# Kernel tuning notes

Measured on AMD Instinct MI355X. Metric: run time of the kernel, lower is better.

The kernel has to match this reference:

```python
import jax, jax.numpy as jnp
import numpy as np

B, C, N, F_, HID = 512, 3, 128, 256, 128  # batch, channels, nodes(=in_dim), num_f(=seq), gru hidden


def setup_inputs() -> dict:
    key = jax.random.key(0)
    ks = jax.random.split(key, 12)
    s = 0.05
    inp = {
        "X": jax.random.normal(ks[0], (B, N, F_), jnp.float32),
        "H": jax.random.uniform(ks[1], (B, C, N, N), jnp.float32),
        "weight": jnp.full((1, 1), 10.0, jnp.float32),        # nn.init.constant_(weight, 10)
        "soft": jnp.full((C,), 1.0 / C, jnp.float32),          # nn.init.constant_(soft, 1/C)
        "w_ih_f": jax.random.normal(ks[2], (3 * HID, N), jnp.float32) * s,
        "w_hh_f": jax.random.normal(ks[3], (3 * HID, HID), jnp.float32) * s,
        "b_ih_f": jax.random.normal(ks[4], (3 * HID,), jnp.float32) * s,
        "b_hh_f": jax.random.normal(ks[5], (3 * HID,), jnp.float32) * s,
        "w_ih_b": jax.random.normal(ks[6], (3 * HID, N), jnp.float32) * s,
        "w_hh_b": jax.random.normal(ks[7], (3 * HID, HID), jnp.float32) * s,
        "b_ih_b": jax.random.normal(ks[8], (3 * HID,), jnp.float32) * s,
        "b_hh_b": jax.random.normal(ks[9], (3 * HID,), jnp.float32) * s,
        "bn_gamma": jnp.ones((F_,), jnp.float32),
        "bn_beta": jnp.zeros((F_,), jnp.float32),
    }
    return inp


def _gru_dir(xs, w_ih, w_hh, b_ih, b_hh):
    # xs: [T, B, in] -> ys: [T, B, HID]; torch GRU cell equations
    def cell(h, x):
        gi = x @ w_ih.T + b_ih
        gh = h @ w_hh.T + b_hh
        i_r, i_z, i_n = jnp.split(gi, 3, axis=-1)
        h_r, h_z, h_n = jnp.split(gh, 3, axis=-1)
        r = jax.nn.sigmoid(i_r + h_r)
        z = jax.nn.sigmoid(i_z + h_z)
        n = jnp.tanh(i_n + r * h_n)
        h_new = (1.0 - z) * n + z * h
        return h_new, h_new
    h0 = jnp.zeros((xs.shape[1], w_hh.shape[1]), xs.dtype)
    _, ys = jax.lax.scan(cell, h0, xs)
    return ys


def reference(X, H, weight, soft, w_ih_f, w_hh_f, b_ih_f, b_hh_f,
              w_ih_b, w_hh_b, b_ih_b, b_hh_b, bn_gamma, bn_beta):
    n = X.shape[1]
    I = jnp.eye(n, dtype=X.dtype)
    # norm(): zero the diagonal, add identity, symmetric D^-1/2 H D^-1/2 (all C channels at once)
    Hn = H * (1.0 - I) + I                              # [B,C,N,N]
    deg = jnp.sum(Hn, axis=-1)                          # [B,C,N]
    dinv = deg ** -0.5
    Hn = dinv[..., :, None] * Hn * dinv[..., None, :]
    # gcn_conv across all features/channels in one einsum; weight is a 1x1 scalar
    HX = jnp.einsum('bcnm,bmf->bcnf', Hn, X) * weight[0, 0]
    Xc = jnp.sum(jax.nn.leaky_relu(HX, 0.01) * soft[None, :, None, None], axis=1)  # [B,N,F]
    # per1 -> [B, F, N]; GRU batch_first with seq_len=F, input=N
    xs = Xc.transpose(2, 0, 1)                          # [T=F, B, N]
    yf = _gru_dir(xs, w_ih_f, w_hh_f, b_ih_f, b_hh_f)
    yb = _gru_dir(xs[::-1], w_ih_b, w_hh_b, b_ih_b, b_hh_b)[::-1]
    y = jnp.concatenate([yf, yb], axis=-1).transpose(1, 0, 2)  # [B, F, 2*HID]

    # BatchNorm1d(num_f), training-mode batch stats over (batch, length) per channel F
    mean = jnp.mean(y, axis=(0, 2), keepdims=True)
    var = jnp.var(y, axis=(0, 2), keepdims=True)
    y = bn_gamma[None, :, None] * (y - mean) / jnp.sqrt(var + 1e-5) + bn_beta[None, :, None]
    # per2 -> [B, 2*HID, F]
    return y.transpose(0, 2, 1)
```

## Files before the change

kernel.cpp:

```cpp
#include <hip/hip_runtime.h>

typedef short s8v  __attribute__((ext_vector_type(8)));
typedef float f4v  __attribute__((ext_vector_type(4)));

#define B_   512
#define C_   3
#define N_   128
#define F_   256
#define T_   256
#define HID_ 128
#define G3_  384

__device__ __forceinline__ ushort f2bf(float f) {
  union { float f; unsigned u; } v; v.f = f;
  return (ushort)((v.u + 0x7FFFu + ((v.u >> 16) & 1u)) >> 16);
}
__device__ __forceinline__ float bf2f(ushort h) {
  union { unsigned u; float f; } v; v.u = ((unsigned)h) << 16;
  return v.f;
}
__device__ __forceinline__ float rcp_(float x) { return __builtin_amdgcn_rcpf(x); }
__device__ __forceinline__ float sigm(float x) { return rcp_(1.0f + __expf(-x)); }
__device__ __forceinline__ float tanh_(float x) { return 2.0f * rcp_(1.0f + __expf(-2.0f * x)) - 1.0f; }

#define LDS_BARRIER() asm volatile("s_waitcnt lgkmcnt(0)\n\ts_barrier" ::: "memory")

__global__ void k_wcvt(const float* __restrict__ a, const float* __restrict__ b,
                       const float* __restrict__ c, const float* __restrict__ d,
                       ushort* __restrict__ o) {
  int i = blockIdx.x * 256 + threadIdx.x;
  const float* src = (i < 49152) ? a : (i < 98304) ? b : (i < 147456) ? c : d;
  o[i] = f2bf(src[i % 49152]);
}

__global__ void k_dinv(const float* __restrict__ H, float* __restrict__ dinv) {
  const int bc = blockIdx.x;
  const int lane = threadIdx.x & 63, w = threadIdx.x >> 6;
  const float* Hm = H + (size_t)bc * N_ * N_;
  for (int r = w * 32; r < w * 32 + 32; ++r) {
    float a = Hm[(size_t)r * N_ + lane];
    float b = Hm[(size_t)r * N_ + 64 + lane];
    if (lane == r) a = 1.0f;
    if (64 + lane == r) b = 1.0f;
    float s = a + b;
    #pragma unroll
    for (int o = 32; o; o >>= 1) s += __shfl_xor(s, o);
    if (lane == 0) dinv[bc * N_ + r] = 1.0f / sqrtf(s);
  }
}

__global__ __launch_bounds__(256, 1) void k_conv(
    const float* __restrict__ X, const float* __restrict__ H,
    const float* __restrict__ dinv, const float* __restrict__ wscal,
    const float* __restrict__ soft, ushort* __restrict__ XcT) {
  __shared__ ushort hn[C_][N_][136];
  __shared__ ushort xt[N_][136];
  __shared__ float dv[C_ * N_];
  const int b = blockIdx.x;
  const int tid = threadIdx.x;
  const int lane = tid & 63, w = tid >> 6;
  const int rq = lane >> 4, l15 = lane & 15;

  for (int i = tid; i < C_ * N_; i += 256) dv[i] = dinv[b * C_ * N_ + i];
  __syncthreads();

  {
    const int m4 = (tid & 31) * 4;
    const int nof = tid >> 5;
    for (int c = 0; c < C_; ++c) {
      const float* Hm = H + ((size_t)(b * C_ + c)) * N_ * N_;
      const float* dvc = dv + c * N_;
      #pragma unroll
      for (int p = 0; p < 16; ++p) {
        int n = p * 8 + nof;
        float4 v = *(const float4*)&Hm[(size_t)n * N_ + m4];
        float f0 = (m4 + 0 == n) ? 1.0f : v.x;
        float f1 = (m4 + 1 == n) ? 1.0f : v.y;
        float f2 = (m4 + 2 == n) ? 1.0f : v.z;
        float f3 = (m4 + 3 == n) ? 1.0f : v.w;
        ushort4 o;
        o.x = f2bf(f0 * dvc[m4 + 0]);
        o.y = f2bf(f1 * dvc[m4 + 1]);
        o.z = f2bf(f2 * dvc[m4 + 2]);
        o.w = f2bf(f3 * dvc[m4 + 3]);
        *(ushort4*)&hn[c][n][m4] = o;
      }
    }
  }

  const float wmul = wscal[0];
  const float scf[3] = {soft[0], soft[1], soft[2]};

  for (int fh = 0; fh < 2; ++fh) {
    __syncthreads();
    {
      const int fl4 = (tid & 31) * 4;
      const int mof = tid >> 5;
      #pragma unroll
      for (int p = 0; p < 16; ++p) {
        int m = p * 8 + mof;
        float4 v = *(const float4*)&X[((size_t)b * N_ + m) * F_ + fh * 128 + fl4];
        xt[fl4 + 0][m] = f2bf(v.x);
        xt[fl4 + 1][m] = f2bf(v.y);
        xt[fl4 + 2][m] = f2bf(v.z);
        xt[fl4 + 3][m] = f2bf(v.w);
      }
    }
    __syncthreads();

    s8v af[2][4];
    #pragma unroll
    for (int rt = 0; rt < 2; ++rt)
      #pragma unroll
      for (int kk = 0; kk < 4; ++kk)
        af[rt][kk] = *(const s8v*)&xt[w * 32 + rt * 16 + l15][kk * 32 + rq * 8];

    f4v xc[2][8];
    #pragma unroll
    for (int rt = 0; rt < 2; ++rt)
      #pragma unroll
      for (int nt = 0; nt < 8; ++nt)
        xc[rt][nt] = (f4v){0.f, 0.f, 0.f, 0.f};

    for (int c = 0; c < C_; ++c) {
      f4v hx[2][8];
      #pragma unroll
      for (int rt = 0; rt < 2; ++rt)
        #pragma unroll
        for (int nt = 0; nt < 8; ++nt)
          hx[rt][nt] = (f4v){0.f, 0.f, 0.f, 0.f};
      #pragma unroll
      for (int kk = 0; kk < 4; ++kk) {
        #pragma unroll
        for (int nt = 0; nt < 8; ++nt) {
          s8v bf = *(const s8v*)&hn[c][nt * 16 + l15][kk * 32 + rq * 8];
          hx[0][nt] = __builtin_amdgcn_mfma_f32_16x16x32_bf16(af[0][kk], bf, hx[0][nt], 0, 0, 0);
          hx[1][nt] = __builtin_amdgcn_mfma_f32_16x16x32_bf16(af[1][kk], bf, hx[1][nt], 0, 0, 0);
        }
      }
      const float* dvc = dv + c * N_;
      const float s = scf[c];
      #pragma unroll
      for (int nt = 0; nt < 8; ++nt) {
        float dn = dvc[nt * 16 + l15] * wmul;
        #pragma unroll
        for (int i = 0; i < 4; ++i) {
          float v0 = hx[0][nt][i] * dn;
          xc[0][nt][i] += s * fmaxf(v0, 0.01f * v0);
          float v1 = hx[1][nt][i] * dn;
          xc[1][nt][i] += s * fmaxf(v1, 0.01f * v1);
        }
      }
    }
    __syncthreads();
    #pragma unroll
    for (int rt = 0; rt < 2; ++rt)
      #pragma unroll
      for (int nt = 0; nt < 8; ++nt)
        #pragma unroll
        for (int i = 0; i < 4; ++i)
          xt[w * 32 + rt * 16 + rq * 4 + i][nt * 16 + l15] = f2bf(xc[rt][nt][i]);
    __syncthreads();
    #pragma unroll
    for (int p = 0; p < 4; ++p) {
      int tl = p * 32 + (tid >> 3);
      int n0 = (tid & 7) * 16;
      size_t rowb = ((size_t)b * F_ + fh * 128 + tl) * N_;
      *(s8v*)&XcT[rowb + n0]     = *(const s8v*)&xt[tl][n0];
      *(s8v*)&XcT[rowb + n0 + 8] = *(const s8v*)&xt[tl][n0 + 8];
    }
  }
}

__global__ __launch_bounds__(512, 2) void k_gru(
    const ushort* __restrict__ XcT, const ushort* __restrict__ wbf,
    const float* __restrict__ bihf, const float* __restrict__ bhhf,
    const float* __restrict__ bihb, const float* __restrict__ bhhb,
    ushort* __restrict__ y) {
  __shared__ ushort hlds[2][16][136];
  __shared__ ushort xbuf[2][16][136];
  const int dir = blockIdx.x >> 5;
  const int chunk = blockIdx.x & 31;
  const int tid = threadIdx.x;
  const int lane = tid & 63, w = tid >> 6;
  const int rq = lane >> 4, l15 = lane & 15;
  const int jb = w * 16;
  const int jr = jb + rq * 4;
  const ushort* wih = wbf + (size_t)(dir * 2) * G3_ * HID_;
  const ushort* whh = wih + G3_ * HID_;
  const float* bih = dir ? bihb : bihf;
  const float* bhh = dir ? bhhb : bhhf;

  s8v fir[4], fiz[4], fin[4], fhr[4], fhz[4], fhn[4];
  #pragma unroll
  for (int kk = 0; kk < 4; ++kk) {
    const int ko = kk * 32 + rq * 8;
    const int row = jb + l15;
    fir[kk] = *(const s8v*)&wih[(size_t)(row)       * HID_ + ko];
    fiz[kk] = *(const s8v*)&wih[(size_t)(128 + row) * HID_ + ko];
    fin[kk] = *(const s8v*)&wih[(size_t)(256 + row) * HID_ + ko];
    fhr[kk] = *(const s8v*)&whh[(size_t)(row)       * HID_ + ko];
    fhz[kk] = *(const s8v*)&whh[(size_t)(128 + row) * HID_ + ko];
    fhn[kk] = *(const s8v*)&whh[(size_t)(256 + row) * HID_ + ko];
  }
  float4 bi_r = *(const float4*)&bih[jr],        bh_r = *(const float4*)&bhh[jr];
  float4 bi_z = *(const float4*)&bih[128 + jr],  bh_z = *(const float4*)&bhh[128 + jr];
  float4 bin4 = *(const float4*)&bih[256 + jr];
  float4 bhn4 = *(const float4*)&bhh[256 + jr];
  f4v br = {bi_r.x + bh_r.x, bi_r.y + bh_r.y, bi_r.z + bh_r.z, bi_r.w + bh_r.w};
  f4v bz = {bi_z.x + bh_z.x, bi_z.y + bh_z.y, bi_z.z + bh_z.z, bi_z.w + bh_z.w};
  f4v bin = {bin4.x, bin4.y, bin4.z, bin4.w};
  f4v bhn = {bhn4.x, bhn4.y, bhn4.z, bhn4.w};

  for (int i = tid; i < 16 * 136; i += 512) ((ushort*)hlds[0])[i] = 0;

  const int rr = tid >> 5;
  const int nq = (tid & 31) * 4;
  const size_t xrow = (size_t)(chunk * 16 + rr) * T_;
  {
    int t0 = dir ? (T_ - 1) : 0;
    *(ushort4*)&xbuf[0][rr][nq] = *(const ushort4*)&XcT[(xrow + t0) * N_ + nq];
  }
  f4v hreg = {0.f, 0.f, 0.f, 0.f};
  __syncthreads();

  for (int s = 0; s < T_; ++s) {
    const int cur = s & 1;
    const int t_in = dir ? (T_ - 1 - s) : s;
    const int sn = (s + 1 < T_) ? s + 1 : s;
    const int t_nx = dir ? (T_ - 1 - sn) : sn;
    ushort4 xn = *(const ushort4*)&XcT[(xrow + t_nx) * N_ + nq];

    f4v ar = br, az = bz, ain = bin, ahn = bhn;
    #pragma unroll
    for (int kk = 0; kk < 4; ++kk) {
      const int ko = kk * 32 + rq * 8;
      s8v xf = *(const s8v*)&xbuf[cur][l15][ko];
      s8v hf = *(const s8v*)&hlds[cur][l15][ko];
      ar  = __builtin_amdgcn_mfma_f32_16x16x32_bf16(fir[kk], xf, ar, 0, 0, 0);
      ar  = __builtin_amdgcn_mfma_f32_16x16x32_bf16(fhr[kk], hf, ar, 0, 0, 0);
      az  = __builtin_amdgcn_mfma_f32_16x16x32_bf16(fiz[kk], xf, az, 0, 0, 0);
      az  = __builtin_amdgcn_mfma_f32_16x16x32_bf16(fhz[kk], hf, az, 0, 0, 0);
      ain = __builtin_amdgcn_mfma_f32_16x16x32_bf16(fin[kk], xf, ain, 0, 0, 0);
      ahn = __builtin_amdgcn_mfma_f32_16x16x32_bf16(fhn[kk], hf, ahn, 0, 0, 0);
    }
    ushort hb[4];
    #pragma unroll
    for (int i = 0; i < 4; ++i) {
      float r = sigm(ar[i]);
      float z = sigm(az[i]);
      float n = tanh_(ain[i] + r * ahn[i]);
      float h = n + z * (hreg[i] - n);
      hreg[i] = h;
      hb[i] = f2bf(h);
    }
    ushort4 hv; hv.x = hb[0]; hv.y = hb[1]; hv.z = hb[2]; hv.w = hb[3];
    *(ushort4*)&y[((size_t)t_in * B_ + chunk * 16 + l15) * 256 + dir * 128 + jr] = hv;
    *(ushort4*)&hlds[cur ^ 1][l15][jr] = hv;
    *(ushort4*)&xbuf[cur ^ 1][rr][nq] = xn;
    LDS_BARRIER();
  }
}

__global__ void k_stats(const ushort* __restrict__ y, const float* __restrict__ gamma,
                        const float* __restrict__ beta, float* __restrict__ stats) {
  const int t = blockIdx.x, tid = threadIdx.x;
  const ushort* p = y + (size_t)t * 256 * B_;
  float s = 0.f, q = 0.f;
  for (int i = tid * 8; i < 256 * B_; i += 256 * 8) {
    s8v v = *(const s8v*)&p[i];
    #pragma unroll
    for (int e = 0; e < 8; ++e) {
      float f = bf2f((ushort)v[e]);
      s += f; q += f * f;
    }
  }
  #pragma unroll
  for (int o = 32; o; o >>= 1) { s += __shfl_xor(s, o); q += __shfl_xor(q, o); }
  __shared__ float rs[4], rq2[4];
  if ((tid & 63) == 0) { rs[tid >> 6] = s; rq2[tid >> 6] = q; }
  __syncthreads();
  if (tid == 0) {
    s = rs[0] + rs[1] + rs[2] + rs[3];
    q = rq2[0] + rq2[1] + rq2[2] + rq2[3];
    const float inv = 1.0f / (256.f * 512.f);
    float mean = s * inv;
    float var = q * inv - mean * mean;
    float istd = 1.0f / sqrtf(var + 1e-5f);
    float a = gamma[t] * istd;
    stats[2 * t] = a;
    stats[2 * t + 1] = beta[t] - mean * a;
  }
}

__global__ __launch_bounds__(256) void k_apply(
    const ushort* __restrict__ y, const float* __restrict__ stats,
    float* __restrict__ out) {
  __shared__ ushort tile[256][64];
  __shared__ float sA[256], sB[256];
  const int b = blockIdx.x;
  const int j0 = blockIdx.y * 64;
  const int tid = threadIdx.x;
  sA[tid] = stats[2 * tid];
  sB[tid] = stats[2 * tid + 1];
  {
    const ushort* src = &y[((size_t)tid * B_ + b) * 256 + j0];
    const int sw = (tid >> 5) & 7;
    #pragma unroll
    for (int q = 0; q < 8; ++q)
      *(s8v*)&tile[tid][(q ^ sw) * 8] = *(const s8v*)&src[q * 8];
  }
  __syncthreads();
  const int j = tid >> 2, jc = j >> 3, jrr = j & 7;
  const int tq = tid & 3;
  float* op = out + ((size_t)b * 256 + j0 + j) * 256 + tq * 64;
  #pragma unroll
  for (int k = 0; k < 16; ++k) {
    const int t = tq * 64 + k * 4;
    float4 o;
    #pragma unroll
    for (int e = 0; e < 4; ++e) {
      const int te = t + e;
      const int sw2 = (te >> 5) & 7;
      const int jcol = ((jc ^ sw2) * 8) + jrr;
      float vv = bf2f(tile[te][jcol]) * sA[te] + sB[te];
      if (e == 0) o.x = vv; else if (e == 1) o.y = vv; else if (e == 2) o.z = vv; else o.w = vv;
    }
    *(float4*)&op[k * 4] = o;
  }
}

extern "C" void kernel_launch(void* const* d_in, const int* in_sizes, int n_in,
                              void* d_out, int out_size, void* d_ws, size_t ws_size,
                              hipStream_t stream) {
  const float* X      = (const float*)d_in[0];
  const float* H      = (const float*)d_in[1];
  const float* weight = (const float*)d_in[2];
  const float* soft   = (const float*)d_in[3];
  const float* w_ih_f = (const float*)d_in[4];
  const float* w_hh_f = (const float*)d_in[5];
  const float* b_ih_f = (const float*)d_in[6];
  const float* b_hh_f = (const float*)d_in[7];
  const float* w_ih_b = (const float*)d_in[8];
  const float* w_hh_b = (const float*)d_in[9];
  const float* b_ih_b = (const float*)d_in[10];
  const float* b_hh_b = (const float*)d_in[11];
  const float* gamma  = (const float*)d_in[12];
  const float* beta   = (const float*)d_in[13];
  float* out = (float*)d_out;

  char* ws = (char*)d_ws;
  ushort* wbf   = (ushort*)(ws);
  float*  dinv  = (float*) (ws + 393216);
  ushort* XcT   = (ushort*)(ws + 1179648);
  ushort* ybuf  = (ushort*)(ws + 34734080);
  float*  stats = (float*) (ws + 101842944);

  k_wcvt<<<768, 256, 0, stream>>>(w_ih_f, w_hh_f, w_ih_b, w_hh_b, wbf);
  k_dinv<<<B_ * C_, 256, 0, stream>>>(H, dinv);
  k_conv<<<B_, 256, 0, stream>>>(X, H, dinv, weight, soft, XcT);
  k_gru<<<64, 512, 0, stream>>>(XcT, wbf, b_ih_f, b_hh_f, b_ih_b, b_hh_b, ybuf);
  k_stats<<<T_, 256, 0, stream>>>(ybuf, gamma, beta, stats);
  k_apply<<<dim3(512, 4), 256, 0, stream>>>(ybuf, stats, out);
}
```

Measured before the change: 403.4 us.

## Restructure GRU kernel to 4 waves with two hidden tiles each and deeper x prefetch

```diff
diff --git a/kernel.cpp b/kernel.cpp
--- a/kernel.cpp
+++ b/kernel.cpp
@@ -172,7 +172,69 @@
   }
 }
 
-__global__ __launch_bounds__(512, 2) void k_gru(
+#define GRU_STEP(SS, CUR, RREG)                                                          \
+  {                                                                                      \
+    const int s = (SS);                                                                  \
+    const int t_in = dir ? (T_ - 1 - s) : s;                                             \
+      \
+    *(s8v*)&xbuf[CUR ^ 1][rr][nq] = RREG;                                                \
+    {                                                                                    \
+      int sp = (s + 3 < T_) ? s + 3 : T_ - 1;                                            \
+      int tp = dir ? (T_ - 1 - sp) : sp;                                                 \
+      RREG = *(const s8v*)&XcT[(xrow + tp) * N_ + nq];                                   \
+    }                                                                                    \
+    s8v xf[4], hf[4];                                                                    \
+    _Pragma("unroll")                                                                    \
+    for (int kk = 0; kk < 4; ++kk) {                                                     \
+      const int ko = kk * 32 + rq * 8;                                                   \
+      xf[kk] = *(const s8v*)&xbuf[CUR][l15][ko];                                         \
+      hf[kk] = *(const s8v*)&hlds[CUR][l15][ko];                                         \
+    }                                                                                    \
+    f4v arx[2], azx[2], anx[2], arh[2], azh[2], ahn[2];                                  \
+    _Pragma("unroll")                                                                    \
+    for (int nt = 0; nt < 2; ++nt) {                                                     \
+      arx[nt] = br[nt]; azx[nt] = bz[nt]; anx[nt] = bin[nt];                             \
+      arh[nt] = (f4v){0.f, 0.f, 0.f, 0.f};                                               \
+      azh[nt] = (f4v){0.f, 0.f, 0.f, 0.f};                                               \
+      ahn[nt] = bhn[nt];                                                                 \
+    }                                                                                    \
+    _Pragma("unroll")                                                                    \
+    for (int kk = 0; kk < 4; ++kk)                                                       \
+      _Pragma("unroll")                                                                  \
+      for (int nt = 0; nt < 2; ++nt) {                                                   \
+        arx[nt] = __builtin_amdgcn_mfma_f32_16x16x32_bf16(fir[nt][kk], xf[kk], arx[nt], 0, 0, 0); \
+        azx[nt] = __builtin_amdgcn_mfma_f32_16x16x32_bf16(fiz[nt][kk], xf[kk], azx[nt], 0, 0, 0); \
+        anx[nt] = __builtin_amdgcn_mfma_f32_16x16x32_bf16(fin[nt][kk], xf[kk], anx[nt], 0, 0, 0); \
+      }                                                                                  \
+    _Pragma("unroll")                                                                    \
+    for (int kk = 0; kk < 4; ++kk)                                                       \
+      _Pragma("unroll")                                                                  \
+      for (int nt = 0; nt < 2; ++nt) {                                                   \
+        arh[nt] = __builtin_amdgcn_mfma_f32_16x16x32_bf16(fhr[nt][kk], hf[kk], arh[nt], 0, 0, 0); \
+        azh[nt] = __builtin_amdgcn_mfma_f32_16x16x32_bf16(fhz[nt][kk], hf[kk], azh[nt], 0, 0, 0); \
+        ahn[nt] = __builtin_amdgcn_mfma_f32_16x16x32_bf16(fhn[nt][kk], hf[kk], ahn[nt], 0, 0, 0); \
+      }                                                                                  \
+    _Pragma("unroll")                                                                    \
+    for (int nt = 0; nt < 2; ++nt) {                                                     \
+      ushort hb[4];                                                                      \
+      _Pragma("unroll")                                                                  \
+      for (int i = 0; i < 4; ++i) {                                                      \
+        float r = sigm(arx[nt][i] + arh[nt][i]);                                         \
+        float z = sigm(azx[nt][i] + azh[nt][i]);                                         \
+        float n = tanh_(anx[nt][i] + r * ahn[nt][i]);                                    \
+        float h = n + z * (hreg[nt][i] - n);                                             \
+        hreg[nt][i] = h;                                                                 \
+        hb[i] = f2bf(h);                                                                 \
+      }                                                                                  \
+      ushort4 hv; hv.x = hb[0]; hv.y = hb[1]; hv.z = hb[2]; hv.w = hb[3];                \
+      const int jj = jb + nt * 16 + rq * 4;                                              \
+      *(ushort4*)&y[((size_t)t_in * B_ + chunk * 16 + l15) * 256 + dir * 128 + jj] = hv; \
+      *(ushort4*)&hlds[CUR ^ 1][l15][jj] = hv;                                           \
+    }                                                                                    \
+    LDS_BARRIER();                                                                       \
+  }
+
+__global__ __launch_bounds__(256, 1) void k_gru(
     const ushort* __restrict__ XcT, const ushort* __restrict__ wbf,
     const float* __restrict__ bihf, const float* __restrict__ bhhf,
     const float* __restrict__ bihb, const float* __restrict__ bhhb,
@@ -184,81 +246,63 @@
   const int tid = threadIdx.x;
   const int lane = tid & 63, w = tid >> 6;
   const int rq = lane >> 4, l15 = lane & 15;
-  const int jb = w * 16;
-  const int jr = jb + rq * 4;
+  const int jb = w * 32;
   const ushort* wih = wbf + (size_t)(dir * 2) * G3_ * HID_;
   const ushort* whh = wih + G3_ * HID_;
   const float* bih = dir ? bihb : bihf;
   const float* bhh = dir ? bhhb : bhhf;
 
-  s8v fir[4], fiz[4], fin[4], fhr[4], fhz[4], fhn[4];
+  s8v fir[2][4], fiz[2][4], fin[2][4], fhr[2][4], fhz[2][4], fhn[2][4];
   #pragma unroll
-  for (int kk = 0; kk < 4; ++kk) {
-    const int ko = kk * 32 + rq * 8;
-    const int row = jb + l15;
-    fir[kk] = *(const s8v*)&wih[(size_t)(row)       * HID_ + ko];
-    fiz[kk] = *(const s8v*)&wih[(size_t)(128 + row) * HID_ + ko];
-    fin[kk] = *(const s8v*)&wih[(size_t)(256 + row) * HID_ + ko];
-    fhr[kk] = *(const s8v*)&whh[(size_t)(row)       * HID_ + ko];
-    fhz[kk] = *(const s8v*)&whh[(size_t)(128 + row) * HID_ + ko];
-    fhn[kk] = *(const s8v*)&whh[(size_t)(256 + row) * HID_ + ko];
-  }
-  float4 bi_r = *(const float4*)&bih[jr],        bh_r = *(const float4*)&bhh[jr];
-  float4 bi_z = *(const float4*)&bih[128 + jr],  bh_z = *(const float4*)&bhh[128 + jr];
-  float4 bin4 = *(const float4*)&bih[256 + jr];
-  float4 bhn4 = *(const float4*)&bhh[256 + jr];
-  f4v br = {bi_r.x + bh_r.x, bi_r.y + bh_r.y, bi_r.z + bh_r.z, bi_r.w + bh_r.w};
-  f4v bz = {bi_z.x + bh_z.x, bi_z.y + bh_z.y, bi_z.z + bh_z.z, bi_z.w + bh_z.w};
-  f4v bin = {bin4.x, bin4.y, bin4.z, bin4.w};
-  f4v bhn = {bhn4.x, bhn4.y, bhn4.z, bhn4.w};
-
-  for (int i = tid; i < 16 * 136; i += 512) ((ushort*)hlds[0])[i] = 0;
-
-  const int rr = tid >> 5;
-  const int nq = (tid & 31) * 4;
+  for (int nt = 0; nt < 2; ++nt)
+    #pragma unroll
+    for (int kk = 0; kk < 4; ++kk) {
+      const int row = jb + nt * 16 + l15;
+      const int ko = kk * 32 + rq * 8;
+      fir[nt][kk] = *(const s8v*)&wih[(size_t)(row)       * HID_ + ko];
+      fiz[nt][kk] = *(const s8v*)&wih[(size_t)(128 + row) * HID_ + ko];
+      fin[nt][kk] = *(const s8v*)&wih[(size_t)(256 + row) * HID_ + ko];
+      fhr[nt][kk] = *(const s8v*)&whh[(size_t)(row)       * HID_ + ko];
+      fhz[nt][kk] = *(const s8v*)&whh[(size_t)(128 + row) * HID_ + ko];
+      fhn[nt][kk] = *(const s8v*)&whh[(size_t)(256 + row) * HID_ + ko];
+    }
+  f4v br[2], bz[2], bin[2], bhn[2];
+  #pragma unroll
+  for (int nt = 0; nt < 2; ++nt) {
+    const int jr = jb + nt * 16 + rq * 4;
+    float4 a1 = *(const float4*)&bih[jr],       a2 = *(const float4*)&bhh[jr];
+    float4 z1 = *(const float4*)&bih[128 + jr], z2 = *(const float4*)&bhh[128 + jr];
+    float4 n1 = *(const float4*)&bih[256 + jr];
+    float4 n2 = *(const float4*)&bhh[256 + jr];
+    br[nt]  = (f4v){a1.x + a2.x, a1.y + a2.y, a1.z + a2.z, a1.w + a2.w};
+    bz[nt]  = (f4v){z1.x + z2.x, z1.y + z2.y, z1.z + z2.z, z1.w + z2.w};
+    bin[nt] = (f4v){n1.x, n1.y, n1.z, n1.w};
+    bhn[nt] = (f4v){n2.x, n2.y, n2.z, n2.w};
+  }
+
+  for (int i = tid; i < 16 * 136; i += 256) ((ushort*)hlds[0])[i] = 0;
+
+  const int rr = tid >> 4;
+  const int nq = (tid & 15) * 8;
   const size_t xrow = (size_t)(chunk * 16 + rr) * T_;
+  s8v R0, R1;
   {
-    int t0 = dir ? (T_ - 1) : 0;
-    *(ushort4*)&xbuf[0][rr][nq] = *(const ushort4*)&XcT[(xrow + t0) * N_ + nq];
-  }
-  f4v hreg = {0.f, 0.f, 0.f, 0.f};
+    const int t0 = dir ? (T_ - 1) : 0;
+    R0 = *(const s8v*)&XcT[(xrow + t0) * N_ + nq];
+    *(s8v*)&xbuf[0][rr][nq] = R0;
+    const int t1 = dir ? (T_ - 2) : 1;
+    R0 = *(const s8v*)&XcT[(xrow + t1) * N_ + nq];
+    const int t2 = dir ? (T_ - 3) : 2;
+    R1 = *(const s8v*)&XcT[(xrow + t2) * N_ + nq];
+  }
+  f4v hreg[2];
+  hreg[0] = (f4v){0.f, 0.f, 0.f, 0.f};
+  hreg[1] = (f4v){0.f, 0.f, 0.f, 0.f};
   __syncthreads();
 
-  for (int s = 0; s < T_; ++s) {
-    const int cur = s & 1;
-    const int t_in = dir ? (T_ - 1 - s) : s;
-    const int sn = (s + 1 < T_) ? s + 1 : s;
-    const int t_nx = dir ? (T_ - 1 - sn) : sn;
-    ushort4 xn = *(const ushort4*)&XcT[(xrow + t_nx) * N_ + nq];
-
-    f4v ar = br, az = bz, ain = bin, ahn = bhn;
-    #pragma unroll
-    for (int kk = 0; kk < 4; ++kk) {
-      const int ko = kk * 32 + rq * 8;
-      s8v xf = *(const s8v*)&xbuf[cur][l15][ko];
-      s8v hf = *(const s8v*)&hlds[cur][l15][ko];
-      ar  = __builtin_amdgcn_mfma_f32_16x16x32_bf16(fir[kk], xf, ar, 0, 0, 0);
-      ar  = __builtin_amdgcn_mfma_f32_16x16x32_bf16(fhr[kk], hf, ar, 0, 0, 0);
-      az  = __builtin_amdgcn_mfma_f32_16x16x32_bf16(fiz[kk], xf, az, 0, 0, 0);
-      az  = __builtin_amdgcn_mfma_f32_16x16x32_bf16(fhz[kk], hf, az, 0, 0, 0);
-      ain = __builtin_amdgcn_mfma_f32_16x16x32_bf16(fin[kk], xf, ain, 0, 0, 0);
-      ahn = __builtin_amdgcn_mfma_f32_16x16x32_bf16(fhn[kk], hf, ahn, 0, 0, 0);
-    }
-    ushort hb[4];
-    #pragma unroll
-    for (int i = 0; i < 4; ++i) {
-      float r = sigm(ar[i]);
-      float z = sigm(az[i]);
-      float n = tanh_(ain[i] + r * ahn[i]);
-      float h = n + z * (hreg[i] - n);
-      hreg[i] = h;
-      hb[i] = f2bf(h);
-    }
-    ushort4 hv; hv.x = hb[0]; hv.y = hb[1]; hv.z = hb[2]; hv.w = hb[3];
-    *(ushort4*)&y[((size_t)t_in * B_ + chunk * 16 + l15) * 256 + dir * 128 + jr] = hv;
-    *(ushort4*)&hlds[cur ^ 1][l15][jr] = hv;
-    *(ushort4*)&xbuf[cur ^ 1][rr][nq] = xn;
-    LDS_BARRIER();
+  for (int s2 = 0; s2 < T_ / 2; ++s2) {
+    GRU_STEP(2 * s2,     0, R0)
+    GRU_STEP(2 * s2 + 1, 1, R1)
   }
 }
 
@@ -359,7 +403,7 @@
   k_wcvt<<<768, 256, 0, stream>>>(w_ih_f, w_hh_f, w_ih_b, w_hh_b, wbf);
   k_dinv<<<B_ * C_, 256, 0, stream>>>(H, dinv);
   k_conv<<<B_, 256, 0, stream>>>(X, H, dinv, weight, soft, XcT);
-  k_gru<<<64, 512, 0, stream>>>(XcT, wbf, b_ih_f, b_hh_f, b_ih_b, b_hh_b, ybuf);
+  k_gru<<<64, 256, 0, stream>>>(XcT, wbf, b_ih_f, b_hh_f, b_ih_b, b_hh_b, ybuf);
   k_stats<<<T_, 256, 0, stream>>>(ybuf, gamma, beta, stats);
   k_apply<<<dim3(512, 4), 256, 0, stream>>>(ybuf, stats, out);
 }
```

New measurement: 499.0 us. +23.7%, slower.

## Precompute GRU input projections in a parallel kernel before the recurrence

Applied to the files above, without the earlier changes.

```diff
diff --git a/kernel.cpp b/kernel.cpp
--- a/kernel.cpp
+++ b/kernel.cpp
@@ -172,7 +172,161 @@
   }
 }
 
-__global__ __launch_bounds__(512, 2) void k_gru(
+__global__ __launch_bounds__(256, 2) void k_gi(
+    const ushort* __restrict__ XcT, const ushort* __restrict__ wbf,
+    const float* __restrict__ bihf, const float* __restrict__ bihb,
+    ushort* __restrict__ gi) {
+  __shared__ ushort xt[128][136];
+  const int b = blockIdx.x;
+  const int dir = blockIdx.y;
+  const int tid = threadIdx.x;
+  const int lane = tid & 63, w = tid >> 6;
+  const int rq = lane >> 4, l15 = lane & 15;
+  const ushort* wih = wbf + (size_t)(dir * 2) * G3_ * HID_;
+  const float* bih = dir ? bihb : bihf;
+  const int chunk = b >> 4, bl = b & 15;
+  const size_t gbase = ((size_t)(dir * 32 + chunk)) * 256 * 16 * 384 + (size_t)bl * 384;
+
+  for (int th = 0; th < 2; ++th) {
+    __syncthreads();
+    {
+      const int tl = tid >> 1;
+      const int n0 = (tid & 1) * 64;
+      const ushort* src = &XcT[((size_t)b * 256 + th * 128 + tl) * 128 + n0];
+      #pragma unroll
+      for (int p = 0; p < 8; ++p)
+        *(s8v*)&xt[tl][n0 + p * 8] = *(const s8v*)&src[p * 8];
+    }
+    __syncthreads();
+
+    for (int gt = w; gt < 24; gt += 4) {
+      const int g0 = gt * 16;
+      s8v wf[4];
+      #pragma unroll
+      for (int kk = 0; kk < 4; ++kk)
+        wf[kk] = *(const s8v*)&wih[(size_t)(g0 + l15) * HID_ + kk * 32 + rq * 8];
+      float4 bi4 = *(const float4*)&bih[g0 + rq * 4];
+      const f4v binit = {bi4.x, bi4.y, bi4.z, bi4.w};
+      #pragma unroll
+      for (int tt = 0; tt < 8; ++tt) {
+        f4v acc = binit;
+        #pragma unroll
+        for (int kk = 0; kk < 4; ++kk) {
+          s8v xf = *(const s8v*)&xt[tt * 16 + l15][kk * 32 + rq * 8];
+          acc = __builtin_amdgcn_mfma_f32_16x16x32_bf16(wf[kk], xf, acc, 0, 0, 0);
+        }
+        const int t = th * 128 + tt * 16 + l15;
+        const int pos = dir ? (T_ - 1 - t) : t;
+        uint2 o;
+        o.x = (unsigned)f2bf(acc[0]) | ((unsigned)f2bf(acc[1]) << 16);
+        o.y = (unsigned)f2bf(acc[2]) | ((unsigned)f2bf(acc[3]) << 16);
+        *(uint2*)&gi[gbase + (size_t)pos * 6144 + g0 + rq * 4] = o;
+      }
+    }
+  }
+}
+
+#define GRUH_STEP(SS, CUR, GR, GZ, GN)                                                    \
+  {                                                                                       \
+    const int s = (SS);                                                                   \
+    const int t_in = dir ? (T_ - 1 - s) : s;                                              \
+    s8v hf[4];                                                                            \
+    _Pragma("unroll")                                                                     \
+    for (int kk = 0; kk < 4; ++kk)                                                        \
+      hf[kk] = *(const s8v*)&hlds[CUR][l15][kk * 32 + rq * 8];                            \
+    f4v ar, az, ahn, gin;                                                                 \
+    ar[0] = bhr[0] + bf2f(GR.x);  ar[1] = bhr[1] + bf2f(GR.y);                            \
+    ar[2] = bhr[2] + bf2f(GR.z);  ar[3] = bhr[3] + bf2f(GR.w);                            \
+    az[0] = bhz[0] + bf2f(GZ.x);  az[1] = bhz[1] + bf2f(GZ.y);                            \
+    az[2] = bhz[2] + bf2f(GZ.z);  az[3] = bhz[3] + bf2f(GZ.w);                            \
+    gin[0] = bf2f(GN.x);  gin[1] = bf2f(GN.y);                                            \
+    gin[2] = bf2f(GN.z);  gin[3] = bf2f(GN.w);                                            \
+    ahn = bhn;                                                                            \
+    _Pragma("unroll")                                                                     \
+    for (int kk = 0; kk < 4; ++kk) {                                                      \
+      ar  = __builtin_amdgcn_mfma_f32_16x16x32_bf16(fhr[kk], hf[kk], ar, 0, 0, 0);        \
+      az  = __builtin_amdgcn_mfma_f32_16x16x32_bf16(fhz[kk], hf[kk], az, 0, 0, 0);        \
+      ahn = __builtin_amdgcn_mfma_f32_16x16x32_bf16(fhn[kk], hf[kk], ahn, 0, 0, 0);       \
+    }                                                                                     \
+    {                                                                                     \
+      int sp = (s + 2 < T_) ? s + 2 : T_ - 1;                                             \
+      const ushort* gp = gib + (size_t)sp * 6144 + l15 * 384 + jr;                        \
+      GR = *(const ushort4*)&gp[0];                                                       \
+      GZ = *(const ushort4*)&gp[128];                                                     \
+      GN = *(const ushort4*)&gp[256];                                                     \
+    }                                                                                     \
+    float hn_[4];                                                                         \
+    _Pragma("unroll")                                                                     \
+    for (int i = 0; i < 4; ++i) {                                                         \
+      float r = sigm(ar[i]);                                                              \
+      float z = sigm(az[i]);                                                              \
+      float n = tanh_(gin[i] + r * ahn[i]);                                               \
+      hn_[i] = n + z * (hreg[i] - n);                                                     \
+      hreg[i] = hn_[i];                                                                   \
+    }                                                                                     \
+    ushort4 hv;                                                                           \
+    hv.x = f2bf(hn_[0]); hv.y = f2bf(hn_[1]);                                             \
+    hv.z = f2bf(hn_[2]); hv.w = f2bf(hn_[3]);                                             \
+    *(ushort4*)&y[((size_t)t_in * B_ + chunk * 16 + l15) * 256 + dir * 128 + jr] = hv;    \
+    *(ushort4*)&hlds[CUR ^ 1][l15][jr] = hv;                                              \
+    LDS_BARRIER();                                                                        \
+  }
+
+__global__ __launch_bounds__(512, 2) void k_gruh(
+    const ushort* __restrict__ gi, const ushort* __restrict__ wbf,
+    const float* __restrict__ bhhf, const float* __restrict__ bhhb,
+    ushort* __restrict__ y) {
+  __shared__ ushort hlds[2][16][136];
+  const int dir = blockIdx.x >> 5;
+  const int chunk = blockIdx.x & 31;
+  const int tid = threadIdx.x;
+  const int lane = tid & 63, w = tid >> 6;
+  const int rq = lane >> 4, l15 = lane & 15;
+  const int jb = w * 16;
+  const int jr = jb + rq * 4;
+  const ushort* whh = wbf + (size_t)(dir * 2) * G3_ * HID_ + G3_ * HID_;
+  const float* bhh = dir ? bhhb : bhhf;
+  const ushort* gib = gi + ((size_t)(dir * 32 + chunk)) * 256 * 6144;
+
+  s8v fhr[4], fhz[4], fhn[4];
+  #pragma unroll
+  for (int kk = 0; kk < 4; ++kk) {
+    const int row = jb + l15;
+    const int ko = kk * 32 + rq * 8;
+    fhr[kk] = *(const s8v*)&whh[(size_t)(row)       * HID_ + ko];
+    fhz[kk] = *(const s8v*)&whh[(size_t)(128 + row) * HID_ + ko];
+    fhn[kk] = *(const s8v*)&whh[(size_t)(256 + row) * HID_ + ko];
+  }
+  float4 r4 = *(const float4*)&bhh[jr];
+  float4 z4 = *(const float4*)&bhh[128 + jr];
+  float4 n4 = *(const float4*)&bhh[256 + jr];
+  const f4v bhr = {r4.x, r4.y, r4.z, r4.w};
+  const f4v bhz = {z4.x, z4.y, z4.z, z4.w};
+  const f4v bhn = {n4.x, n4.y, n4.z, n4.w};
+
+  for (int i = tid; i < 16 * 136; i += 512) ((ushort*)hlds[0])[i] = 0;
+
+  ushort4 GR0, GZ0, GN0, GR1, GZ1, GN1;
+  {
+    const ushort* g0p = gib + (size_t)0 * 6144 + l15 * 384 + jr;
+    GR0 = *(const ushort4*)&g0p[0];
+    GZ0 = *(const ushort4*)&g0p[128];
+    GN0 = *(const ushort4*)&g0p[256];
+    const ushort* g1p = gib + (size_t)1 * 6144 + l15 * 384 + jr;
+    GR1 = *(const ushort4*)&g1p[0];
+    GZ1 = *(const ushort4*)&g1p[128];
+    GN1 = *(const ushort4*)&g1p[256];
+  }
+  f4v hreg = {0.f, 0.f, 0.f, 0.f};
+  __syncthreads();
+
+  for (int s2 = 0; s2 < T_ / 2; ++s2) {
+    GRUH_STEP(2 * s2,     0, GR0, GZ0, GN0)
+    GRUH_STEP(2 * s2 + 1, 1, GR1, GZ1, GN1)
+  }
+}
+
+__global__ __launch_bounds__(512, 2) void k_gru_fb(
     const ushort* __restrict__ XcT, const ushort* __restrict__ wbf,
     const float* __restrict__ bihf, const float* __restrict__ bhhf,
     const float* __restrict__ bihb, const float* __restrict__ bhhb,
@@ -355,11 +509,18 @@
   ushort* XcT   = (ushort*)(ws + 1179648);
   ushort* ybuf  = (ushort*)(ws + 34734080);
   float*  stats = (float*) (ws + 101842944);
+  ushort* gibuf = (ushort*)(ws + 101846016);
+  const size_t NEED = 101846016ull + 201326592ull;
 
   k_wcvt<<<768, 256, 0, stream>>>(w_ih_f, w_hh_f, w_ih_b, w_hh_b, wbf);
   k_dinv<<<B_ * C_, 256, 0, stream>>>(H, dinv);
   k_conv<<<B_, 256, 0, stream>>>(X, H, dinv, weight, soft, XcT);
-  k_gru<<<64, 512, 0, stream>>>(XcT, wbf, b_ih_f, b_hh_f, b_ih_b, b_hh_b, ybuf);
+  if (ws_size >= NEED) {
+    k_gi<<<dim3(512, 2), 256, 0, stream>>>(XcT, wbf, b_ih_f, b_ih_b, gibuf);
+    k_gruh<<<64, 512, 0, stream>>>(gibuf, wbf, b_hh_f, b_hh_b, ybuf);
+  } else {
+    k_gru_fb<<<64, 512, 0, stream>>>(XcT, wbf, b_ih_f, b_hh_f, b_ih_b, b_hh_b, ybuf);
+  }
   k_stats<<<T_, 256, 0, stream>>>(ybuf, gamma, beta, stats);
   k_apply<<<dim3(512, 4), 256, 0, stream>>>(ybuf, stats, out);
 }
```

Measured after the change: 532.1 us. 31.9% more time.

## Fuse degree normalization into conv kernel and weight conversion into GRU

Applied to the files above, without the earlier changes.

```diff
diff --git a/kernel.cpp b/kernel.cpp
--- a/kernel.cpp
+++ b/kernel.cpp
@@ -23,36 +23,23 @@
 __device__ __forceinline__ float sigm(float x) { return rcp_(1.0f + __expf(-x)); }
 __device__ __forceinline__ float tanh_(float x) { return 2.0f * rcp_(1.0f + __expf(-2.0f * x)) - 1.0f; }
 
+__device__ __forceinline__ s8v ld8cvt(const float* p) {
+  float4 a = *(const float4*)p;
+  float4 b = *(const float4*)(p + 4);
+  s8v r;
+  r[0] = (short)f2bf(a.x); r[1] = (short)f2bf(a.y);
+  r[2] = (short)f2bf(a.z); r[3] = (short)f2bf(a.w);
+  r[4] = (short)f2bf(b.x); r[5] = (short)f2bf(b.y);
+  r[6] = (short)f2bf(b.z); r[7] = (short)f2bf(b.w);
+  return r;
+}
+
 #define LDS_BARRIER() asm volatile("s_waitcnt lgkmcnt(0)\n\ts_barrier" ::: "memory")
-
-__global__ void k_wcvt(const float* __restrict__ a, const float* __restrict__ b,
-                       const float* __restrict__ c, const float* __restrict__ d,
-                       ushort* __restrict__ o) {
-  int i = blockIdx.x * 256 + threadIdx.x;
-  const float* src = (i < 49152) ? a : (i < 98304) ? b : (i < 147456) ? c : d;
-  o[i] = f2bf(src[i % 49152]);
-}
-
-__global__ void k_dinv(const float* __restrict__ H, float* __restrict__ dinv) {
-  const int bc = blockIdx.x;
-  const int lane = threadIdx.x & 63, w = threadIdx.x >> 6;
-  const float* Hm = H + (size_t)bc * N_ * N_;
-  for (int r = w * 32; r < w * 32 + 32; ++r) {
-    float a = Hm[(size_t)r * N_ + lane];
-    float b = Hm[(size_t)r * N_ + 64 + lane];
-    if (lane == r) a = 1.0f;
-    if (64 + lane == r) b = 1.0f;
-    float s = a + b;
-    #pragma unroll
-    for (int o = 32; o; o >>= 1) s += __shfl_xor(s, o);
-    if (lane == 0) dinv[bc * N_ + r] = 1.0f / sqrtf(s);
-  }
-}
 
 __global__ __launch_bounds__(256, 1) void k_conv(
     const float* __restrict__ X, const float* __restrict__ H,
-    const float* __restrict__ dinv, const float* __restrict__ wscal,
-    const float* __restrict__ soft, ushort* __restrict__ XcT) {
+    const float* __restrict__ wscal, const float* __restrict__ soft,
+    ushort* __restrict__ XcT) {
   __shared__ ushort hn[C_][N_][136];
   __shared__ ushort xt[N_][136];
   __shared__ float dv[C_ * N_];
@@ -61,15 +48,11 @@
   const int lane = tid & 63, w = tid >> 6;
   const int rq = lane >> 4, l15 = lane & 15;
 
-  for (int i = tid; i < C_ * N_; i += 256) dv[i] = dinv[b * C_ * N_ + i];
-  __syncthreads();
-
   {
     const int m4 = (tid & 31) * 4;
     const int nof = tid >> 5;
     for (int c = 0; c < C_; ++c) {
       const float* Hm = H + ((size_t)(b * C_ + c)) * N_ * N_;
-      const float* dvc = dv + c * N_;
       #pragma unroll
       for (int p = 0; p < 16; ++p) {
         int n = p * 8 + nof;
@@ -79,10 +62,31 @@
         float f2 = (m4 + 2 == n) ? 1.0f : v.z;
         float f3 = (m4 + 3 == n) ? 1.0f : v.w;
         ushort4 o;
-        o.x = f2bf(f0 * dvc[m4 + 0]);
-        o.y = f2bf(f1 * dvc[m4 + 1]);
-        o.z = f2bf(f2 * dvc[m4 + 2]);
-        o.w = f2bf(f3 * dvc[m4 + 3]);
+        o.x = f2bf(f0); o.y = f2bf(f1); o.z = f2bf(f2); o.w = f2bf(f3);
+        *(ushort4*)&hn[c][n][m4] = o;
+        float s = (f0 + f1) + (f2 + f3);
+        #pragma unroll
+        for (int off = 16; off; off >>= 1) s += __shfl_xor(s, off);
+        if ((tid & 31) == 0) dv[c * N_ + n] = 1.0f / sqrtf(s);
+      }
+    }
+  }
+  __syncthreads();
+  {
+    const int m4 = (tid & 31) * 4;
+    const int nof = tid >> 5;
+    for (int c = 0; c < C_; ++c) {
+      const float* dvc = dv + c * N_;
+      float d0 = dvc[m4 + 0], d1 = dvc[m4 + 1], d2 = dvc[m4 + 2], d3 = dvc[m4 + 3];
+      #pragma unroll
+      for (int p = 0; p < 16; ++p) {
+        int n = p * 8 + nof;
+        ushort4 h4 = *(const ushort4*)&hn[c][n][m4];
+        ushort4 o;
+        o.x = f2bf(bf2f(h4.x) * d0);
+        o.y = f2bf(bf2f(h4.y) * d1);
+        o.z = f2bf(bf2f(h4.z) * d2);
+        o.w = f2bf(bf2f(h4.w) * d3);
         *(ushort4*)&hn[c][n][m4] = o;
       }
     }
@@ -173,8 +177,10 @@
 }
 
 __global__ __launch_bounds__(512, 2) void k_gru(
-    const ushort* __restrict__ XcT, const ushort* __restrict__ wbf,
+    const ushort* __restrict__ XcT,
+    const float* __restrict__ wihf, const float* __restrict__ whhf,
     const float* __restrict__ bihf, const float* __restrict__ bhhf,
+    const float* __restrict__ wihb, const float* __restrict__ whhb,
     const float* __restrict__ bihb, const float* __restrict__ bhhb,
     ushort* __restrict__ y) {
   __shared__ ushort hlds[2][16][136];
@@ -186,8 +192,8 @@
   const int rq = lane >> 4, l15 = lane & 15;
   const int jb = w * 16;
   const int jr = jb + rq * 4;
-  const ushort* wih = wbf + (size_t)(dir * 2) * G3_ * HID_;
-  const ushort* whh = wih + G3_ * HID_;
+  const float* wih = dir ? wihb : wihf;
+  const float* whh = dir ? whhb : whhf;
   const float* bih = dir ? bihb : bihf;
   const float* bhh = dir ? bhhb : bhhf;
 
@@ -196,12 +202,12 @@
   for (int kk = 0; kk < 4; ++kk) {
     const int ko = kk * 32 + rq * 8;
     const int row = jb + l15;
-    fir[kk] = *(const s8v*)&wih[(size_t)(row)       * HID_ + ko];
-    fiz[kk] = *(const s8v*)&wih[(size_t)(128 + row) * HID_ + ko];
-    fin[kk] = *(const s8v*)&wih[(size_t)(256 + row) * HID_ + ko];
-    fhr[kk] = *(const s8v*)&whh[(size_t)(row)       * HID_ + ko];
-    fhz[kk] = *(const s8v*)&whh[(size_t)(128 + row) * HID_ + ko];
-    fhn[kk] = *(const s8v*)&whh[(size_t)(256 + row) * HID_ + ko];
+    fir[kk] = ld8cvt(&wih[(size_t)(row)       * HID_ + ko]);
+    fiz[kk] = ld8cvt(&wih[(size_t)(128 + row) * HID_ + ko]);
+    fin[kk] = ld8cvt(&wih[(size_t)(256 + row) * HID_ + ko]);
+    fhr[kk] = ld8cvt(&whh[(size_t)(row)       * HID_ + ko]);
+    fhz[kk] = ld8cvt(&whh[(size_t)(128 + row) * HID_ + ko]);
+    fhn[kk] = ld8cvt(&whh[(size_t)(256 + row) * HID_ + ko]);
   }
   float4 bi_r = *(const float4*)&bih[jr],        bh_r = *(const float4*)&bhh[jr];
   float4 bi_z = *(const float4*)&bih[128 + jr],  bh_z = *(const float4*)&bhh[128 + jr];
@@ -350,16 +356,13 @@
   float* out = (float*)d_out;
 
   char* ws = (char*)d_ws;
-  ushort* wbf   = (ushort*)(ws);
-  float*  dinv  = (float*) (ws + 393216);
-  ushort* XcT   = (ushort*)(ws + 1179648);
-  ushort* ybuf  = (ushort*)(ws + 34734080);
-  float*  stats = (float*) (ws + 101842944);
-
-  k_wcvt<<<768, 256, 0, stream>>>(w_ih_f, w_hh_f, w_ih_b, w_hh_b, wbf);
-  k_dinv<<<B_ * C_, 256, 0, stream>>>(H, dinv);
-  k_conv<<<B_, 256, 0, stream>>>(X, H, dinv, weight, soft, XcT);
-  k_gru<<<64, 512, 0, stream>>>(XcT, wbf, b_ih_f, b_hh_f, b_ih_b, b_hh_b, ybuf);
+  ushort* XcT   = (ushort*)(ws);
+  ushort* ybuf  = (ushort*)(ws + 33554432);
+  float*  stats = (float*) (ws + 100663296);
+
+  k_conv<<<B_, 256, 0, stream>>>(X, H, weight, soft, XcT);
+  k_gru<<<64, 512, 0, stream>>>(XcT, w_ih_f, w_hh_f, b_ih_f, b_hh_f,
+                                w_ih_b, w_hh_b, b_ih_b, b_hh_b, ybuf);
   k_stats<<<T_, 256, 0, stream>>>(ybuf, gamma, beta, stats);
   k_apply<<<dim3(512, 4), 256, 0, stream>>>(ybuf, stats, out);
 }
```

After: 423.1 us. +4.9%, slower.
